# Kernel optimization log

Measured on AMD Instinct MI355X. Metric: run time of the kernel, lower is better.

Reference implementation:

```python
import jax, jax.numpy as jnp
import numpy as np

N_NODES = 50000
N_EDGES = 800000
F_IN = 256
HID = 64
HEADS = 4
NEG_SLOPE = 0.2


def setup_inputs() -> dict:
    key = jax.random.key(0)
    ks = jax.random.split(key, 12)
    x = jax.random.normal(ks[0], (N_NODES, F_IN), dtype=jnp.float32)
    src = jax.random.randint(ks[1], (N_EDGES,), 0, N_NODES)
    dst = jax.random.randint(ks[2], (N_EDGES,), 0, N_NODES)
    s0 = 1.0 / np.sqrt(F_IN)
    s1 = 1.0 / np.sqrt(HEADS * HID)
    W0 = jax.random.normal(ks[3], (F_IN, HEADS * HID), dtype=jnp.float32) * s0
    a_l0 = jax.random.normal(ks[4], (HEADS, HID), dtype=jnp.float32) * s1
    a_r0 = jax.random.normal(ks[5], (HEADS, HID), dtype=jnp.float32) * s1
    b0 = jnp.zeros((HEADS * HID,), dtype=jnp.float32)
    W1 = jax.random.normal(ks[6], (HEADS * HID, HEADS * HID), dtype=jnp.float32) * s1
    a_l1 = jax.random.normal(ks[7], (HEADS, HID), dtype=jnp.float32) * s1
    a_r1 = jax.random.normal(ks[8], (HEADS, HID), dtype=jnp.float32) * s1
    b1 = jnp.zeros((HEADS * HID,), dtype=jnp.float32)
    return {"x": x, "src": src, "dst": dst,
            "W0": W0, "a_l0": a_l0, "a_r0": a_r0, "b0": b0,
            "W1": W1, "a_l1": a_l1, "a_r1": a_r1, "b1": b1}


def _gat_layer(h, src, dst, W, a_l, a_r, b):
    # h: [N, F_in] -> feat: [N, H, D]
    feat = (h @ W).reshape(h.shape[0], HEADS, HID)
    el = jnp.sum(feat * a_l, axis=-1)  # [N, H]
    er = jnp.sum(feat * a_r, axis=-1)  # [N, H]
    e = jax.nn.leaky_relu(el[src] + er[dst], NEG_SLOPE)  # [E, H]
    # per-destination edge softmax (numerically stable)
    m = jax.ops.segment_max(e, dst, num_segments=N_NODES)  # [N, H]
    ex = jnp.exp(e - m[dst])
    s = jax.ops.segment_sum(ex, dst, num_segments=N_NODES)  # [N, H]
    alpha = ex / jnp.maximum(s[dst], 1e-9)  # [E, H]
    msg = feat[src] * alpha[:, :, None]  # [E, H, D]
    rst = jax.ops.segment_sum(msg, dst, num_segments=N_NODES)  # [N, H, D]
    rst = rst + b.reshape(1, HEADS, HID)
    return jax.nn.elu(rst)


def reference(x, src, dst, W0, a_l0, a_r0, b0, W1, a_l1, a_r1, b1):
    h = _gat_layer(x, src, dst, W0, a_l0, a_r0, b0)  # [N, H, D]
    h = h.reshape(N_NODES, HEADS * HID)              # flatten(1)
    h = _gat_layer(h, src, dst, W1, a_l1, a_r1, b1)  # [N, H, D]
    # list of per-head outputs h[:, i]
    return tuple(h[:, i] for i in range(HEADS))
```

## Files before the change

kernel.cpp:

```cpp
#include <hip/hip_runtime.h>
#include <math.h>

#define N_NODES 50000
#define N_EDGES 800000
#define HEADS 4
#define HID 64
#define FDIM 256
#define LDA 40
#define SCAN_CHUNK 1024
#define SCAN_NB ((N_NODES + SCAN_CHUNK - 1) / SCAN_CHUNK)

typedef __attribute__((ext_vector_type(8))) _Float16 half8;
typedef __attribute__((ext_vector_type(4))) _Float16 half4;
typedef __attribute__((ext_vector_type(4))) float f32x4;


__global__ __launch_bounds__(256) void hist_kernel(const int* __restrict__ dst,
                                                   int* __restrict__ counts, int E) {
    int i = blockIdx.x * blockDim.x + threadIdx.x;
    if (i < E) atomicAdd(&counts[dst[i]], 1);
}

__global__ __launch_bounds__(256) void scan_local(const int* __restrict__ counts,
                                                  int* __restrict__ offs,
                                                  int* __restrict__ bsum, int n) {
    __shared__ int part[256];
    const int b = blockIdx.x, t = threadIdx.x;
    const int base = b * SCAN_CHUNK + t * 4;
    int v[4];
#pragma unroll
    for (int j = 0; j < 4; j++) {
        int idx = base + j;
        v[j] = (idx < n) ? counts[idx] : 0;
    }
    int s0 = v[0], s1 = s0 + v[1], s2 = s1 + v[2], s3 = s2 + v[3];
    part[t] = s3;
    __syncthreads();
    for (int off = 1; off < 256; off <<= 1) {
        int x = (t >= off) ? part[t - off] : 0;
        __syncthreads();
        part[t] += x;
        __syncthreads();
    }
    int prefix = (t > 0) ? part[t - 1] : 0;
    int e[4] = {prefix, prefix + s0, prefix + s1, prefix + s2};
#pragma unroll
    for (int j = 0; j < 4; j++) {
        int idx = base + j;
        if (idx < n) offs[idx] = e[j];
    }
    if (t == 255) bsum[b] = part[255];
}

__global__ __launch_bounds__(64) void scan_bsum(int* __restrict__ bsum,
                                                int* __restrict__ offs, int nb, int n) {
    int lane = threadIdx.x;
    int own = (lane < nb) ? bsum[lane] : 0;
    int v = own;
    for (int off = 1; off < 64; off <<= 1) {
        int x = __shfl_up(v, off);
        if (lane >= off) v += x;
    }
    if (lane < nb) bsum[lane] = v - own;
    if (lane == nb - 1) offs[n] = v;
}

__global__ __launch_bounds__(256) void scan_add(int* __restrict__ offs,
                                                const int* __restrict__ bsum, int n) {
    const int b = blockIdx.x;
    const int p = bsum[b];
    const int base = b * SCAN_CHUNK + threadIdx.x * 4;
#pragma unroll
    for (int j = 0; j < 4; j++) {
        int idx = base + j;
        if (idx < n) offs[idx] += p;
    }
}

__global__ __launch_bounds__(256) void scatter_kernel(const int* __restrict__ src,
                                                      const int* __restrict__ dst,
                                                      const int* __restrict__ offs,
                                                      int* __restrict__ cursor,
                                                      int* __restrict__ csr_src, int E) {
    int i = blockIdx.x * blockDim.x + threadIdx.x;
    if (i < E) {
        int d = dst[i];
        int p = offs[d] + atomicAdd(&cursor[d], 1);
        csr_src[p] = src[i];
    }
}


__global__ __launch_bounds__(256) void wcast_kernel(const float* __restrict__ W0,
                                                    const float* __restrict__ W1,
                                                    _Float16* __restrict__ wt0,
                                                    _Float16* __restrict__ wt1) {
    const float* W = blockIdx.y ? W1 : W0;
    _Float16* wt = blockIdx.y ? wt1 : wt0;
    int n = blockIdx.x * 16 + (threadIdx.x >> 4);
    int k0 = (threadIdx.x & 15) * 16;
    for (int j = 0; j < 16; j++)
        wt[n * FDIM + k0 + j] = (_Float16)W[(k0 + j) * FDIM + n];
}

template <int A32>
__global__ __launch_bounds__(512) void mfma_gemm(const _Float16* __restrict__ A16,
                                                 const float* __restrict__ Af,
                                                 const _Float16* __restrict__ Bt,
                                                 const float* __restrict__ al,
                                                 const float* __restrict__ ar,
                                                 _Float16* __restrict__ feat16,
                                                 float* __restrict__ el,
                                                 float* __restrict__ er) {
    __shared__ _Float16 ash[128][LDA];
    __shared__ _Float16 bsh[256][LDA];

    const int t = threadIdx.x;
    const int m0 = blockIdx.x * 128;
    const int wave = t >> 6, lane = t & 63;
    const int quad = lane >> 4, l16 = lane & 15;
    const int wr = (wave >> 2) * 64;
    const int wc = (wave & 3) * 64;

    const f32x4 zero = {0.f, 0.f, 0.f, 0.f};
    f32x4 acc[4][4];
#pragma unroll
    for (int i = 0; i < 4; i++)
#pragma unroll
        for (int j = 0; j < 4; j++) acc[i][j] = zero;

    for (int kk = 0; kk < FDIM; kk += 32) {
        {
            int row = t >> 2;
            int kb = (t & 3) * 8;
            int gr = m0 + row; if (gr >= N_NODES) gr = N_NODES - 1;
            if (A32) {
                const float* p = &Af[(size_t)gr * FDIM + kk + kb];
                float4 f0 = *(const float4*)p;
                float4 f1 = *(const float4*)(p + 4);
                half8 hv = {(_Float16)f0.x, (_Float16)f0.y, (_Float16)f0.z, (_Float16)f0.w,
                            (_Float16)f1.x, (_Float16)f1.y, (_Float16)f1.z, (_Float16)f1.w};
                *(half8*)&ash[row][kb] = hv;
            } else {
                *(half8*)&ash[row][kb] = *(const half8*)&A16[(size_t)gr * FDIM + kk + kb];
            }
        }
#pragma unroll
        for (int ii = 0; ii < 2; ii++) {
            int idx = t + ii * 512;
            int row = idx >> 2;
            int kb = (idx & 3) * 8;
            *(half8*)&bsh[row][kb] = *(const half8*)&Bt[(size_t)row * FDIM + kk + kb];
        }
        __syncthreads();

        half8 af[4], bf[4];
#pragma unroll
        for (int i = 0; i < 4; i++) {
            af[i] = *(half8*)&ash[wr + i * 16 + l16][quad * 8];
            bf[i] = *(half8*)&bsh[wc + i * 16 + l16][quad * 8];
        }
#pragma unroll
        for (int mt = 0; mt < 4; mt++)
#pragma unroll
            for (int nt = 0; nt < 4; nt++)
                acc[mt][nt] = __builtin_amdgcn_mfma_f32_16x16x32_f16(af[mt], bf[nt], acc[mt][nt], 0, 0, 0);
        __syncthreads();
    }

    const int h = wc >> 6;
    float alv[4], arv[4];
#pragma unroll
    for (int nt = 0; nt < 4; nt++) {
        alv[nt] = al[wc + nt * 16 + l16];
        arv[nt] = ar[wc + nt * 16 + l16];
    }
#pragma unroll
    for (int mt = 0; mt < 4; mt++) {
        int m = m0 + wr + mt * 16 + quad * 4;
        float pl[4] = {0.f, 0.f, 0.f, 0.f}, pr[4] = {0.f, 0.f, 0.f, 0.f};
#pragma unroll
        for (int nt = 0; nt < 4; nt++) {
            int n = wc + nt * 16 + l16;
#pragma unroll
            for (int r = 0; r < 4; r++) {
                float v = acc[mt][nt][r];
                if (m + r < N_NODES) feat16[(size_t)(m + r) * FDIM + n] = (_Float16)v;
                pl[r] += v * alv[nt];
                pr[r] += v * arv[nt];
            }
        }
#pragma unroll
        for (int r = 0; r < 4; r++) {
            float a = pl[r], b = pr[r];
            for (int off = 8; off; off >>= 1) {
                a += __shfl_down(a, off, 16);
                b += __shfl_down(b, off, 16);
            }
            if (l16 == 0 && m + r < N_NODES) {
                el[(m + r) * 4 + h] = a;
                er[(m + r) * 4 + h] = b;
            }
        }
    }
}

__global__ __launch_bounds__(256) void agg_fused(const _Float16* __restrict__ feat16,
                                                 const float* __restrict__ el,
                                                 const float* __restrict__ er,
                                                 const float* __restrict__ bias,
                                                 const int* __restrict__ offs,
                                                 const int* __restrict__ csr_src,
                                                 float* __restrict__ out,
                                                 _Float16* __restrict__ h1,
                                                 int mode) {
    const int wave = threadIdx.x >> 6;
    const int lane = threadIdx.x & 63;
    const int n = blockIdx.x * 4 + wave;
    const int head = lane >> 4;
    const int f = lane * 4;
    const int base16 = lane & 48;
    const int j16 = lane & 15;
    const int beg = offs[n];
    const int end = offs[n + 1];
    const float er_h = er[n * 4 + head];

    float4 acc = make_float4(0.f, 0.f, 0.f, 0.f);
    float ss = 0.f;

    for (int c = beg; c < end; c += 16) {
        int e = c + j16;
        int s_own = 0;
        float w_own = 0.f;
        if (e < end) {
            s_own = csr_src[e];
            float lg = el[s_own * 4 + head] + er_h;
            lg = (lg > 0.f) ? lg : 0.2f * lg;
            w_own = __expf(lg);
        }
        ss += w_own;

        int rem = end - c;
        if (rem > 16) rem = 16;

        int j = 0;
        for (; j + 3 < rem; j += 4) {
            int s0 = __shfl(s_own, base16 + j);
            int s1 = __shfl(s_own, base16 + j + 1);
            int s2 = __shfl(s_own, base16 + j + 2);
            int s3 = __shfl(s_own, base16 + j + 3);
            float w0 = __shfl(w_own, base16 + j);
            float w1 = __shfl(w_own, base16 + j + 1);
            float w2 = __shfl(w_own, base16 + j + 2);
            float w3 = __shfl(w_own, base16 + j + 3);
            half4 v0 = *(const half4*)&feat16[(size_t)s0 * FDIM + f];
            half4 v1 = *(const half4*)&feat16[(size_t)s1 * FDIM + f];
            half4 v2 = *(const half4*)&feat16[(size_t)s2 * FDIM + f];
            half4 v3 = *(const half4*)&feat16[(size_t)s3 * FDIM + f];
            acc.x += w0 * (float)v0[0] + w1 * (float)v1[0];
            acc.y += w0 * (float)v0[1] + w1 * (float)v1[1];
            acc.z += w0 * (float)v0[2] + w1 * (float)v1[2];
            acc.w += w0 * (float)v0[3] + w1 * (float)v1[3];
            acc.x += w2 * (float)v2[0] + w3 * (float)v3[0];
            acc.y += w2 * (float)v2[1] + w3 * (float)v3[1];
            acc.z += w2 * (float)v2[2] + w3 * (float)v3[2];
            acc.w += w2 * (float)v2[3] + w3 * (float)v3[3];
        }
        for (; j < rem; j++) {
            int s0 = __shfl(s_own, base16 + j);
            float w0 = __shfl(w_own, base16 + j);
            half4 v0 = *(const half4*)&feat16[(size_t)s0 * FDIM + f];
            acc.x += w0 * (float)v0[0];
            acc.y += w0 * (float)v0[1];
            acc.z += w0 * (float)v0[2];
            acc.w += w0 * (float)v0[3];
        }
    }

    ss += __shfl_xor(ss, 1, 16);
    ss += __shfl_xor(ss, 2, 16);
    ss += __shfl_xor(ss, 4, 16);
    ss += __shfl_xor(ss, 8, 16);

    float S = fmaxf(ss, 1e-9f);
    float inv = 1.f / S;
    float4 bv = *(const float4*)&bias[f];
    float r0 = acc.x * inv + bv.x;
    float r1 = acc.y * inv + bv.y;
    float r2 = acc.z * inv + bv.z;
    float r3 = acc.w * inv + bv.w;
    r0 = (r0 > 0.f) ? r0 : expm1f(r0);
    r1 = (r1 > 0.f) ? r1 : expm1f(r1);
    r2 = (r2 > 0.f) ? r2 : expm1f(r2);
    r3 = (r3 > 0.f) ? r3 : expm1f(r3);

    if (mode) {
        const int d = (lane & 15) * 4;
        float4 rv = make_float4(r0, r1, r2, r3);
        *(float4*)&out[(size_t)head * N_NODES * HID + (size_t)n * HID + d] = rv;
    } else {
        half4 hv = {(_Float16)r0, (_Float16)r1, (_Float16)r2, (_Float16)r3};
        *(half4*)&h1[(size_t)n * FDIM + f] = hv;
    }
}


extern "C" void kernel_launch(void* const* d_in, const int* in_sizes, int n_in,
                              void* d_out, int out_size, void* d_ws, size_t ws_size,
                              hipStream_t stream) {
    const float* x   = (const float*)d_in[0];
    const int*   src = (const int*)d_in[1];
    const int*   dst = (const int*)d_in[2];
    const float* W0  = (const float*)d_in[3];
    const float* al0 = (const float*)d_in[4];
    const float* ar0 = (const float*)d_in[5];
    const float* b0  = (const float*)d_in[6];
    const float* W1  = (const float*)d_in[7];
    const float* al1 = (const float*)d_in[8];
    const float* ar1 = (const float*)d_in[9];
    const float* b1  = (const float*)d_in[10];
    float* out = (float*)d_out;

    _Float16* h1 = (_Float16*)d_out;

    _Float16* feat16 = (_Float16*)d_ws;
    _Float16* wt0 = feat16 + (size_t)N_NODES * FDIM;
    _Float16* wt1 = wt0 + FDIM * FDIM;
    float* el    = (float*)(wt1 + FDIM * FDIM);
    float* er    = el + N_NODES * HEADS;
    int* counts  = (int*)(er + N_NODES * HEADS);
    int* cursor  = counts + N_NODES;
    int* offs    = cursor + N_NODES;
    int* bsum    = offs + 50016;
    int* csr_src = bsum + 64;

    hipMemsetAsync(counts, 0, 2 * N_NODES * sizeof(int), stream);
    wcast_kernel<<<dim3(16, 2), 256, 0, stream>>>(W0, W1, wt0, wt1);
    hist_kernel<<<(N_EDGES + 255) / 256, 256, 0, stream>>>(dst, counts, N_EDGES);
    scan_local<<<SCAN_NB, 256, 0, stream>>>(counts, offs, bsum, N_NODES);
    scan_bsum<<<1, 64, 0, stream>>>(bsum, offs, SCAN_NB, N_NODES);
    scan_add<<<SCAN_NB, 256, 0, stream>>>(offs, bsum, N_NODES);
    scatter_kernel<<<(N_EDGES + 255) / 256, 256, 0, stream>>>(src, dst, offs, cursor, csr_src, N_EDGES);

    const int ggrid = (N_NODES + 127) / 128;

    mfma_gemm<1><<<ggrid, 512, 0, stream>>>(nullptr, x, wt0, al0, ar0, feat16, el, er);
    agg_fused<<<N_NODES / 4, 256, 0, stream>>>(feat16, el, er, b0, offs, csr_src,
                                               out, h1, 0);

    mfma_gemm<0><<<ggrid, 512, 0, stream>>>(h1, nullptr, wt1, al1, ar1, feat16, el, er);
    agg_fused<<<N_NODES / 4, 256, 0, stream>>>(feat16, el, er, b1, offs, csr_src,
                                               out, h1, 1);
}
```

Measured before the change: 378.9 us.

## Fuse CSR build and weight cast into one cooperative kernel with grid syncs

Replaces the memset, weight-cast, histogram, three scan kernels and scatter with a single cooperative kernel of 1024 blocks that separates phases with grid-wide syncs. This removes six launch boundaries and the memset. The cost is five grid.sync barriers, and the histogram and scatter work runs on a fixed, smaller grid using grid-stride loops. The weight transpose-cast is now element-per-thread with strided reads.

```diff
diff --git a/kernel.cpp b/kernel.cpp
--- a/kernel.cpp
+++ b/kernel.cpp
@@ -1,5 +1,8 @@
 #include <hip/hip_runtime.h>
+#include <hip/hip_cooperative_groups.h>
 #include <math.h>
+
+namespace cg = cooperative_groups;
 
 #define N_NODES 50000
 #define N_EDGES 800000
@@ -9,98 +12,100 @@
 #define LDA 40
 #define SCAN_CHUNK 1024
 #define SCAN_NB ((N_NODES + SCAN_CHUNK - 1) / SCAN_CHUNK)
+#define COOP_BLOCKS 1024
 
 typedef __attribute__((ext_vector_type(8))) _Float16 half8;
 typedef __attribute__((ext_vector_type(4))) _Float16 half4;
 typedef __attribute__((ext_vector_type(4))) float f32x4;
 
-
-__global__ __launch_bounds__(256) void hist_kernel(const int* __restrict__ dst,
-                                                   int* __restrict__ counts, int E) {
-    int i = blockIdx.x * blockDim.x + threadIdx.x;
-    if (i < E) atomicAdd(&counts[dst[i]], 1);
-}
-
-__global__ __launch_bounds__(256) void scan_local(const int* __restrict__ counts,
-                                                  int* __restrict__ offs,
-                                                  int* __restrict__ bsum, int n) {
+__global__ __launch_bounds__(256) void build_all(const int* __restrict__ src,
+                                                 const int* __restrict__ dst,
+                                                 const float* __restrict__ W0,
+                                                 const float* __restrict__ W1,
+                                                 _Float16* __restrict__ wt0,
+                                                 _Float16* __restrict__ wt1,
+                                                 int* __restrict__ counts,
+                                                 int* __restrict__ cursor,
+                                                 int* __restrict__ offs,
+                                                 int* __restrict__ bsum,
+                                                 int* __restrict__ csr_src) {
+    cg::grid_group grid = cg::this_grid();
+    const int b = blockIdx.x, tt = threadIdx.x;
+    const int t = b * 256 + tt;
+    const int NT = gridDim.x * 256;
     __shared__ int part[256];
-    const int b = blockIdx.x, t = threadIdx.x;
-    const int base = b * SCAN_CHUNK + t * 4;
-    int v[4];
-#pragma unroll
-    for (int j = 0; j < 4; j++) {
-        int idx = base + j;
-        v[j] = (idx < n) ? counts[idx] : 0;
-    }
-    int s0 = v[0], s1 = s0 + v[1], s2 = s1 + v[2], s3 = s2 + v[3];
-    part[t] = s3;
-    __syncthreads();
-    for (int off = 1; off < 256; off <<= 1) {
-        int x = (t >= off) ? part[t - off] : 0;
+
+    for (int i = t; i < N_NODES; i += NT) { counts[i] = 0; cursor[i] = 0; }
+    for (int i = t; i < 2 * FDIM * FDIM; i += NT) {
+        int which = i >> 16;
+        int rem = i & 65535;
+        int n = rem >> 8, k = rem & 255;
+        const float* W = which ? W1 : W0;
+        _Float16* wt = which ? wt1 : wt0;
+        wt[n * FDIM + k] = (_Float16)W[k * FDIM + n];
+    }
+    grid.sync();
+
+    for (int i = t; i < N_EDGES; i += NT) atomicAdd(&counts[dst[i]], 1);
+    grid.sync();
+
+    const int base = b * SCAN_CHUNK + tt * 4;
+    int s0_ = 0, s1_ = 0, s2_ = 0, s3_ = 0;
+    if (b < SCAN_NB) {
+        int v[4];
+#pragma unroll
+        for (int j = 0; j < 4; j++) {
+            int idx = base + j;
+            v[j] = (idx < N_NODES) ? counts[idx] : 0;
+        }
+        s0_ = v[0]; s1_ = s0_ + v[1]; s2_ = s1_ + v[2]; s3_ = s2_ + v[3];
+        part[tt] = s3_;
         __syncthreads();
-        part[t] += x;
-        __syncthreads();
-    }
-    int prefix = (t > 0) ? part[t - 1] : 0;
-    int e[4] = {prefix, prefix + s0, prefix + s1, prefix + s2};
-#pragma unroll
-    for (int j = 0; j < 4; j++) {
-        int idx = base + j;
-        if (idx < n) offs[idx] = e[j];
-    }
-    if (t == 255) bsum[b] = part[255];
-}
-
-__global__ __launch_bounds__(64) void scan_bsum(int* __restrict__ bsum,
-                                                int* __restrict__ offs, int nb, int n) {
-    int lane = threadIdx.x;
-    int own = (lane < nb) ? bsum[lane] : 0;
-    int v = own;
-    for (int off = 1; off < 64; off <<= 1) {
-        int x = __shfl_up(v, off);
-        if (lane >= off) v += x;
-    }
-    if (lane < nb) bsum[lane] = v - own;
-    if (lane == nb - 1) offs[n] = v;
-}
-
-__global__ __launch_bounds__(256) void scan_add(int* __restrict__ offs,
-                                                const int* __restrict__ bsum, int n) {
-    const int b = blockIdx.x;
-    const int p = bsum[b];
-    const int base = b * SCAN_CHUNK + threadIdx.x * 4;
-#pragma unroll
-    for (int j = 0; j < 4; j++) {
-        int idx = base + j;
-        if (idx < n) offs[idx] += p;
-    }
-}
-
-__global__ __launch_bounds__(256) void scatter_kernel(const int* __restrict__ src,
-                                                      const int* __restrict__ dst,
-                                                      const int* __restrict__ offs,
-                                                      int* __restrict__ cursor,
-                                                      int* __restrict__ csr_src, int E) {
-    int i = blockIdx.x * blockDim.x + threadIdx.x;
-    if (i < E) {
+        for (int off = 1; off < 256; off <<= 1) {
+            int x = (tt >= off) ? part[tt - off] : 0;
+            __syncthreads();
+            part[tt] += x;
+            __syncthreads();
+        }
+        int prefix = (tt > 0) ? part[tt - 1] : 0;
+        int ev[4] = {prefix, prefix + s0_, prefix + s1_, prefix + s2_};
+#pragma unroll
+        for (int j = 0; j < 4; j++) {
+            int idx = base + j;
+            if (idx < N_NODES) offs[idx] = ev[j];
+        }
+        if (tt == 255) bsum[b] = part[255];
+    }
+    grid.sync();
+
+    if (b == 0 && tt < 64) {
+        int lane = tt;
+        int own = (lane < SCAN_NB) ? bsum[lane] : 0;
+        int v = own;
+        for (int off = 1; off < 64; off <<= 1) {
+            int x = __shfl_up(v, off);
+            if (lane >= off) v += x;
+        }
+        if (lane < SCAN_NB) bsum[lane] = v - own;
+        if (lane == SCAN_NB - 1) offs[N_NODES] = v;
+    }
+    grid.sync();
+
+    if (b < SCAN_NB) {
+        int p = bsum[b];
+#pragma unroll
+        for (int j = 0; j < 4; j++) {
+            int idx = base + j;
+            if (idx < N_NODES) offs[idx] += p;
+        }
+    }
+    grid.sync();
+
+    for (int i = t; i < N_EDGES; i += NT) {
         int d = dst[i];
         int p = offs[d] + atomicAdd(&cursor[d], 1);
         csr_src[p] = src[i];
     }
-}
-
-
-__global__ __launch_bounds__(256) void wcast_kernel(const float* __restrict__ W0,
-                                                    const float* __restrict__ W1,
-                                                    _Float16* __restrict__ wt0,
-                                                    _Float16* __restrict__ wt1) {
-    const float* W = blockIdx.y ? W1 : W0;
-    _Float16* wt = blockIdx.y ? wt1 : wt0;
-    int n = blockIdx.x * 16 + (threadIdx.x >> 4);
-    int k0 = (threadIdx.x & 15) * 16;
-    for (int j = 0; j < 16; j++)
-        wt[n * FDIM + k0 + j] = (_Float16)W[(k0 + j) * FDIM + n];
 }
 
 template <int A32>
@@ -334,13 +339,13 @@
     int* bsum    = offs + 50016;
     int* csr_src = bsum + 64;
 
-    hipMemsetAsync(counts, 0, 2 * N_NODES * sizeof(int), stream);
-    wcast_kernel<<<dim3(16, 2), 256, 0, stream>>>(W0, W1, wt0, wt1);
-    hist_kernel<<<(N_EDGES + 255) / 256, 256, 0, stream>>>(dst, counts, N_EDGES);
-    scan_local<<<SCAN_NB, 256, 0, stream>>>(counts, offs, bsum, N_NODES);
-    scan_bsum<<<1, 64, 0, stream>>>(bsum, offs, SCAN_NB, N_NODES);
-    scan_add<<<SCAN_NB, 256, 0, stream>>>(offs, bsum, N_NODES);
-    scatter_kernel<<<(N_EDGES + 255) / 256, 256, 0, stream>>>(src, dst, offs, cursor, csr_src, N_EDGES);
+    {
+        void* args[] = {(void*)&src, (void*)&dst, (void*)&W0, (void*)&W1,
+                        (void*)&wt0, (void*)&wt1, (void*)&counts, (void*)&cursor,
+                        (void*)&offs, (void*)&bsum, (void*)&csr_src};
+        hipLaunchCooperativeKernel((const void*)build_all, dim3(COOP_BLOCKS),
+                                   dim3(256), args, 0, stream);
+    }
 
     const int ggrid = (N_NODES + 127) / 128;
 
```

New measurement: 926.7 us. 2.45x slower.
